# Kernel optimization log

Hardware: AMD Instinct MI355X
Metric: run time of the kernel (lower is better)

Reference implementation:

```python
import jax, jax.numpy as jnp
import numpy as np
from jax import lax

B, L, H = 2, 1024, 1024
D = 2048          # intermediate_size
N = 16            # ssm state size
K = 4             # conv kernel
R = 64            # time_step_rank


def setup_inputs() -> dict:
    key = jax.random.key(0)
    ks = jax.random.split(key, 10)
    def nrm(k, shape, scale=0.02):
        return jax.random.normal(k, shape, dtype=jnp.float32) * scale
    A = jnp.arange(1, N + 1, dtype=jnp.float32)[None, :] * jnp.ones((D, 1), jnp.float32)
    return {
        "hidden_states": jax.random.normal(ks[0], (B, L, H), dtype=jnp.float32),
        "W_in":  nrm(ks[1], (2 * D, H)),
        "conv_w": nrm(ks[2], (D, 1, K), 0.1),
        "conv_b": nrm(ks[3], (D,), 0.1),
        "W_x":   nrm(ks[4], (R + 2 * N, D)),
        "W_dt":  nrm(ks[5], (D, R), 0.1),
        "b_dt":  jnp.full((D,), -4.6, jnp.float32),  # softplus(-4.6) ~ 0.01 dt init
        "A_log": jnp.log(A),
        "D_param": jnp.ones((D,), jnp.float32),
        "W_out": nrm(ks[6], (H, D)),
    }


def _mamba_forward(hidden_states, W_in, conv_w, conv_b, W_x, W_dt, b_dt, A_log, D_param, W_out):
    silu = jax.nn.silu
    # in_proj -> [B, L, 2D], chunk into x and gate
    proj = jnp.einsum("blh,eh->ble", hidden_states, W_in)
    x, gate = jnp.split(proj, 2, axis=-1)           # [B,L,D] each
    # depthwise causal conv over time: [B,D,L]
    xc = x.swapaxes(1, 2)
    xc = lax.conv_general_dilated(
        xc, conv_w, window_strides=(1,), padding=[(K - 1, 0)],
        dimension_numbers=("NCH", "OIH", "NCH"), feature_group_count=D)
    x = silu(xc + conv_b[None, :, None]).swapaxes(1, 2)   # [B,L,D]
    # x_proj -> dt, Bmat, Cmat
    ssm_p = jnp.einsum("bld,rd->blr", x, W_x)             # [B,L,R+2N]
    dt_lr, Bm, Cm = ssm_p[..., :R], ssm_p[..., R:R + N], ssm_p[..., R + N:]
    dt = jax.nn.softplus(jnp.einsum("blr,dr->bld", dt_lr, W_dt) + b_dt)  # [B,L,D]
    A = -jnp.exp(A_log)                                   # [D,N]
    dA = jnp.exp(dt[..., None] * A[None, None])           # [B,L,D,N]
    dBu = dt[..., None] * Bm[:, :, None, :] * x[..., None]  # [B,L,D,N]
    # selective scan over time
    def step(h, inp):
        dA_t, dBu_t, C_t = inp                            # [B,D,N],[B,D,N],[B,N]
        h = dA_t * h + dBu_t
        y = jnp.einsum("bdn,bn->bd", h, C_t)
        return h, y
    h0 = jnp.zeros((B, D, N), dt.dtype)
    _, ys = lax.scan(step, h0, (dA.swapaxes(0, 1), dBu.swapaxes(0, 1), Cm.swapaxes(0, 1)))
    y = ys.swapaxes(0, 1)                                 # [B,L,D]
    y = (y + x * D_param[None, None, :]) * silu(gate)
    return jnp.einsum("bld,hd->blh", y, W_out)            # [B,L,H]


def reference(hidden_states, W_in, conv_w, conv_b, W_x, W_dt, b_dt, A_log, D_param, W_out):
    return _mamba_forward(hidden_states, W_in, conv_w, conv_b, W_x, W_dt, b_dt, A_log, D_param, W_out)
```

## Files before the change

kernel.cpp:

```cpp
#include <hip/hip_runtime.h>
#include <hip/hip_bf16.h>
#include <math.h>

#define B_ 2
#define L_ 1024
#define H_ 1024
#define D_ 2048
#define N_ 16
#define R_ 64
#define NCK 32
#define CL 32

typedef short short8 __attribute__((ext_vector_type(8)));
typedef float floatx4 __attribute__((ext_vector_type(4)));

__device__ __forceinline__ float siluf(float g) {
    return g / (1.0f + __expf(-g));
}

__device__ __forceinline__ unsigned short f2bf(float f) {
    unsigned int u = __float_as_uint(f);
    u = (u + 0x7fffu + ((u >> 16) & 1u)) >> 16;
    return (unsigned short)u;
}

__device__ __forceinline__ float bf2f(unsigned short u) {
    return __uint_as_float(((unsigned int)u) << 16);
}

__device__ __forceinline__ void gl2lds(const unsigned short* g, unsigned short* l) {
    __builtin_amdgcn_global_load_lds(
        (const __attribute__((address_space(1))) unsigned int*)g,
        (__attribute__((address_space(3))) unsigned int*)l, 16, 0, 0);
}

#define Q0 524288
#define Q1 1572864
#define Q2 2097152
#define Q3 2146304
#define Q4 2179072
__global__ __launch_bounds__(256) void cvt_all(
    const float* __restrict__ i0, const float* __restrict__ i1,
    const float* __restrict__ i2, const float* __restrict__ i3,
    const float* __restrict__ i4,
    unsigned short* __restrict__ o0, unsigned short* __restrict__ o1,
    unsigned short* __restrict__ o2, unsigned short* __restrict__ o3,
    unsigned short* __restrict__ o4)
{
    int q = blockIdx.x * 256 + threadIdx.x;
    if (q >= Q4) return;
    const float* in; unsigned short* out; int base;
    if (q < Q0)      { in = i0; out = o0; base = 0; }
    else if (q < Q1) { in = i1; out = o1; base = Q0; }
    else if (q < Q2) { in = i2; out = o2; base = Q1; }
    else if (q < Q3) { in = i3; out = o3; base = Q2; }
    else             { in = i4; out = o4; base = Q3; }
    int i = (q - base) * 4;
    float4 v = *(const float4*)(in + i);
    ushort4 o;
    o.x = f2bf(v.x); o.y = f2bf(v.y); o.z = f2bf(v.z); o.w = f2bf(v.w);
    *(ushort4*)(out + i) = o;
}

template<int EPI>
__global__ __launch_bounds__(256) void gemm_bf16_nt(
    const unsigned short* __restrict__ A, const unsigned short* __restrict__ Bm,
    float* __restrict__ C, int K, int Ncols, int ldc, int kChunk, int nMax,
    size_t partStride, unsigned short* __restrict__ C2)
{
    __shared__ unsigned short As[128 * 32];
    __shared__ unsigned short Bs[128 * 32];
    const int tid  = threadIdx.x;
    const int lane = tid & 63;
    const int wave = tid >> 6;
    const int wm = (wave >> 1) * 64;
    const int wn = (wave & 1) * 64;
    const int lr   = lane & 15;
    const int quad = lane >> 4;
    const int m0 = blockIdx.y * 128;
    const int n0 = blockIdx.x * 128;
    const int k0 = blockIdx.z * kChunk;

    const int srow = wave * 32 + (lane >> 2);
    const int sq   = (lane & 3) * 8;
    unsigned short* AsB0 = &As[(wave * 32) * 32];
    unsigned short* AsB1 = &As[(wave * 32 + 16) * 32];
    unsigned short* BsB0 = &Bs[(wave * 32) * 32];
    unsigned short* BsB1 = &Bs[(wave * 32 + 16) * 32];
    const size_t aoff0 = (size_t)(m0 + srow) * K + sq;
    const size_t aoff1 = (size_t)(m0 + srow + 16) * K + sq;
    const size_t boff0 = (size_t)min(n0 + srow, nMax - 1) * K + sq;
    const size_t boff1 = (size_t)min(n0 + srow + 16, nMax - 1) * K + sq;

    floatx4 acc[4][4];
#pragma unroll
    for (int mi = 0; mi < 4; ++mi)
#pragma unroll
        for (int ni = 0; ni < 4; ++ni)
            acc[mi][ni] = (floatx4){0.f, 0.f, 0.f, 0.f};

    for (int kt = k0; kt < k0 + kChunk; kt += 32) {
        __syncthreads();
        gl2lds(A + aoff0 + kt, AsB0);
        gl2lds(A + aoff1 + kt, AsB1);
        gl2lds(Bm + boff0 + kt, BsB0);
        gl2lds(Bm + boff1 + kt, BsB1);
        __syncthreads();
        short8 af[4], bf[4];
#pragma unroll
        for (int mi = 0; mi < 4; ++mi)
            af[mi] = *(const short8*)&As[(wm + mi * 16 + lr) * 32 + quad * 8];
#pragma unroll
        for (int ni = 0; ni < 4; ++ni)
            bf[ni] = *(const short8*)&Bs[(wn + ni * 16 + lr) * 32 + quad * 8];
#pragma unroll
        for (int mi = 0; mi < 4; ++mi)
#pragma unroll
            for (int ni = 0; ni < 4; ++ni)
                acc[mi][ni] = __builtin_amdgcn_mfma_f32_16x16x32_bf16(
                    af[mi], bf[ni], acc[mi][ni], 0, 0, 0);
    }

    if constexpr (EPI == 4) {
        if (n0 < 2048) {
            __shared__ unsigned short Ct[2 * 64 * 136];
            unsigned short* Cb = (unsigned short*)C;
            unsigned short* Cw = &Ct[(wave & 1) * 64 * 136];
#pragma unroll
            for (int mi = 0; mi < 4; ++mi)
#pragma unroll
                for (int ni = 0; ni < 4; ++ni) {
                    const int ccl = ni * 16 + lr;
                    const int rrl = wm + mi * 16 + quad * 4;
                    ushort4 v;
                    v.x = f2bf(acc[mi][ni][0]);
                    v.y = f2bf(acc[mi][ni][1]);
                    v.z = f2bf(acc[mi][ni][2]);
                    v.w = f2bf(acc[mi][ni][3]);
                    *(ushort4*)&Cw[ccl * 136 + rrl] = v;
                }
            __syncthreads();
            const int row = tid >> 2;
            const int mq = (tid & 3) * 32;
#pragma unroll
            for (int h = 0; h < 2; ++h) {
                const unsigned short* src = &Ct[h * 64 * 136 + row * 136 + mq];
                uint4 w0 = *(const uint4*)(src);
                uint4 w1 = *(const uint4*)(src + 8);
                uint4 w2 = *(const uint4*)(src + 16);
                uint4 w3 = *(const uint4*)(src + 24);
                unsigned short* dst = Cb + (size_t)(n0 + h * 64 + row) * 2048 + m0 + mq;
                *(uint4*)dst = w0;
                *(uint4*)(dst + 8) = w1;
                *(uint4*)(dst + 16) = w2;
                *(uint4*)(dst + 24) = w3;
            }
        } else {
#pragma unroll
            for (int mi = 0; mi < 4; ++mi)
#pragma unroll
                for (int ni = 0; ni < 4; ++ni) {
                    const int rr = m0 + wm + mi * 16 + quad * 4;
                    const int cc = n0 + wn + ni * 16 + lr - 2048;
#pragma unroll
                    for (int r = 0; r < 4; ++r)
                        C2[(size_t)(rr + r) * 2048 + cc] = f2bf(acc[mi][ni][r]);
                }
        }
    } else {
        float* Cz = C + (size_t)blockIdx.z * partStride;
#pragma unroll
        for (int mi = 0; mi < 4; ++mi)
#pragma unroll
            for (int ni = 0; ni < 4; ++ni) {
                const int rr = m0 + wm + mi * 16 + quad * 4;
                const int cc = n0 + wn + ni * 16 + lr;
                if (cc >= Ncols) continue;
#pragma unroll
                for (int r = 0; r < 4; ++r)
                    Cz[(size_t)(rr + r) * ldc + cc] = acc[mi][ni][r];
            }
    }
}

__global__ __launch_bounds__(256) void reduce_ssm(
    const float* __restrict__ P, float* __restrict__ ssm_p,
    unsigned short* __restrict__ sp64)
{
    const int q = blockIdx.x * 256 + threadIdx.x;
    const int m = q / 24;
    const int c = (q - m * 24) * 4;
    const size_t idx = (size_t)m * 96 + c;
    float4 s = make_float4(0.f, 0.f, 0.f, 0.f);
#pragma unroll
    for (int z = 0; z < 16; ++z) {
        float4 v = *(const float4*)(P + (size_t)z * (2048 * 96) + idx);
        s.x += v.x; s.y += v.y; s.z += v.z; s.w += v.w;
    }
    *(float4*)(ssm_p + idx) = s;
    if (c < 64) {
        ushort4 o;
        o.x = f2bf(s.x); o.y = f2bf(s.y); o.z = f2bf(s.z); o.w = f2bf(s.w);
        *(ushort4*)(sp64 + (size_t)m * 64 + c) = o;
    }
}

__global__ __launch_bounds__(256) void reduce_out(
    const float* __restrict__ P, float* __restrict__ out)
{
    const size_t i = ((size_t)blockIdx.x * 256 + threadIdx.x) * 4;
    float4 a = *(const float4*)(P + i);
    float4 b = *(const float4*)(P + 2097152 + i);
    float4 c = *(const float4*)(P + 2 * 2097152 + i);
    float4 d = *(const float4*)(P + 3 * 2097152 + i);
    *(float4*)(out + i) = make_float4(a.x + b.x + c.x + d.x,
                                      a.y + b.y + c.y + d.y,
                                      a.z + b.z + c.z + d.z,
                                      a.w + b.w + c.w + d.w);
}

__global__ __launch_bounds__(256) void dt_gemm(
    const unsigned short* __restrict__ A,
    const unsigned short* __restrict__ Bm,
    unsigned short* __restrict__ C,
    const float* __restrict__ bias)
{
    __shared__ unsigned short As[64 * 72];
    __shared__ unsigned short Bs[64 * 72];
    const int tid = threadIdx.x;
    const int lane = tid & 63;
    const int wave = tid >> 6;
    const int lr = lane & 15;
    const int quad = lane >> 4;
    const int n0 = blockIdx.x * 64;
    const int m0 = blockIdx.y * 64;

    {
        const int row = tid >> 3;
        const int cq = (tid & 7) * 8;
        uint4 a0 = *(const uint4*)(A + (size_t)(m0 + row) * 64 + cq);
        uint4 a1 = *(const uint4*)(A + (size_t)(m0 + 32 + row) * 64 + cq);
        uint4 b0 = *(const uint4*)(Bm + (size_t)(n0 + row) * 64 + cq);
        uint4 b1 = *(const uint4*)(Bm + (size_t)(n0 + 32 + row) * 64 + cq);
        *(uint4*)&As[row * 72 + cq] = a0;
        *(uint4*)&As[(32 + row) * 72 + cq] = a1;
        *(uint4*)&Bs[row * 72 + cq] = b0;
        *(uint4*)&Bs[(32 + row) * 72 + cq] = b1;
    }
    __syncthreads();

    floatx4 acc[4];
#pragma unroll
    for (int ni = 0; ni < 4; ++ni) acc[ni] = (floatx4){0.f, 0.f, 0.f, 0.f};

#pragma unroll
    for (int kt = 0; kt < 64; kt += 32) {
        short8 af = *(const short8*)&As[(wave * 16 + lr) * 72 + kt + quad * 8];
#pragma unroll
        for (int ni = 0; ni < 4; ++ni) {
            short8 bf = *(const short8*)&Bs[(ni * 16 + lr) * 72 + kt + quad * 8];
            acc[ni] = __builtin_amdgcn_mfma_f32_16x16x32_bf16(af, bf, acc[ni], 0, 0, 0);
        }
    }

    const int rr = m0 + wave * 16 + quad * 4;
#pragma unroll
    for (int ni = 0; ni < 4; ++ni) {
        const int cc = n0 + ni * 16 + lr;
        const float bv = bias[cc];
#pragma unroll
        for (int r = 0; r < 4; ++r) {
            const float z = acc[ni][r] + bv;
            const float spv = fmaxf(z, 0.f) + __logf(1.f + __expf(-fabsf(z)));
            C[(size_t)(rr + r) * 2048 + cc] = f2bf(spv);
        }
    }
}

__global__ __launch_bounds__(256) void conv_silu_kernel(
    const unsigned short* __restrict__ projx, const float* __restrict__ conv_w,
    const float* __restrict__ conv_b, unsigned short* __restrict__ x_bf)
{
    __shared__ unsigned short tile[64][72];
    const int t = threadIdx.x;
    const int d0 = blockIdx.x * 64;
    const int lt0 = blockIdx.y * 64;
    const int b = blockIdx.z;
    const int dl = t & 63;
    const int seg = t >> 6;
    const int d = d0 + dl;
    const int l0 = lt0 + seg * 16;
    const unsigned short* row = projx + (size_t)d * 2048 + b * 1024;
    const float w0 = conv_w[d * 4 + 0], w1 = conv_w[d * 4 + 1];
    const float w2 = conv_w[d * 4 + 2], w3 = conv_w[d * 4 + 3];
    const float bias = conv_b[d];

    float p[19];
    p[0] = (l0 >= 3) ? bf2f(row[l0 - 3]) : 0.f;
    p[1] = (l0 >= 2) ? bf2f(row[l0 - 2]) : 0.f;
    p[2] = (l0 >= 1) ? bf2f(row[l0 - 1]) : 0.f;
    {
        short8 q0 = *(const short8*)(row + l0);
        short8 q1 = *(const short8*)(row + l0 + 8);
#pragma unroll
        for (int j = 0; j < 8; ++j) {
            p[3 + j] = bf2f((unsigned short)q0[j]);
            p[11 + j] = bf2f((unsigned short)q1[j]);
        }
    }
#pragma unroll
    for (int j = 0; j < 16; ++j) {
        float v = siluf(bias + w0 * p[j] + w1 * p[j + 1] + w2 * p[j + 2] + w3 * p[j + 3]);
        tile[seg * 16 + j][dl] = f2bf(v);
    }
    __syncthreads();

    const int ml = t >> 2;
    const int c = t & 3;
    short8 s0 = *(const short8*)&tile[ml][c * 16];
    short8 s1 = *(const short8*)&tile[ml][c * 16 + 8];
    unsigned short* dst = x_bf + (size_t)(b * 1024 + lt0 + ml) * 2048 + d0 + c * 16;
    *(short8*)dst = s0;
    *(short8*)(dst + 8) = s1;
}

__global__ __launch_bounds__(256) void scan_p1(
    const unsigned short* __restrict__ dt, const unsigned short* __restrict__ x_bf,
    const float* __restrict__ sp, const float* __restrict__ A_log,
    float* __restrict__ Pch, float* __restrict__ Hch)
{
    __shared__ float sB[CL][16];
    const int tid = threadIdx.x;
    const int d = blockIdx.x * 256 + tid;
    const int ck = blockIdx.y;
    const int b = blockIdx.z;
    const int mb = b * 1024 + ck * CL;

    if (tid < CL * 4) {
        int row = tid >> 2, q = (tid & 3) * 4;
        *(float4*)&sB[row][q] = *(const float4*)(sp + (size_t)(mb + row) * 96 + 64 + q);
    }
    float An2[16];
    {
        const float* al = A_log + d * 16;
#pragma unroll
        for (int j = 0; j < 16; j += 4) {
            float4 a4 = *(const float4*)(al + j);
            An2[j + 0] = -__expf(a4.x) * 1.44269504f;
            An2[j + 1] = -__expf(a4.y) * 1.44269504f;
            An2[j + 2] = -__expf(a4.z) * 1.44269504f;
            An2[j + 3] = -__expf(a4.w) * 1.44269504f;
        }
    }
    __syncthreads();

    float h[16];
#pragma unroll
    for (int n = 0; n < 16; ++n) h[n] = 0.f;
    float dts = 0.f;

    for (int l = 0; l < CL; ++l) {
        const size_t off = (size_t)(mb + l) * 2048 + d;
        const float dtv = bf2f(dt[off]);
        const float xv = bf2f(x_bf[off]);
        const float u = dtv * xv;
        dts += dtv;
        float4 B0 = *(const float4*)&sB[l][0];
        float4 B1 = *(const float4*)&sB[l][4];
        float4 B2 = *(const float4*)&sB[l][8];
        float4 B3 = *(const float4*)&sB[l][12];
        float Bv[16] = {B0.x, B0.y, B0.z, B0.w, B1.x, B1.y, B1.z, B1.w,
                        B2.x, B2.y, B2.z, B2.w, B3.x, B3.y, B3.z, B3.w};
#pragma unroll
        for (int n = 0; n < 16; ++n) {
            const float dA = __builtin_amdgcn_exp2f(dtv * An2[n]);
            h[n] = fmaf(dA, h[n], Bv[n] * u);
        }
    }

    const size_t base = ((size_t)(b * NCK + ck) * 2048 + d) * 16;
#pragma unroll
    for (int j = 0; j < 16; j += 4) {
        float4 pv = make_float4(__builtin_amdgcn_exp2f(dts * An2[j]),
                                __builtin_amdgcn_exp2f(dts * An2[j + 1]),
                                __builtin_amdgcn_exp2f(dts * An2[j + 2]),
                                __builtin_amdgcn_exp2f(dts * An2[j + 3]));
        *(float4*)(Pch + base + j) = pv;
        *(float4*)(Hch + base + j) = make_float4(h[j], h[j + 1], h[j + 2], h[j + 3]);
    }
}

__global__ __launch_bounds__(256) void scan_combine(
    float* __restrict__ Pch, const float* __restrict__ Hch)
{
    const int flat = blockIdx.x * 256 + threadIdx.x;
    const int dn = flat & 32767;
    const int b = flat >> 15;
    float hin = 0.f;
#pragma unroll 4
    for (int ck = 0; ck < NCK; ++ck) {
        const size_t a = ((size_t)(b * NCK + ck) << 15) + dn;
        const float p = Pch[a];
        const float hc = Hch[a];
        Pch[a] = hin;
        hin = fmaf(p, hin, hc);
    }
}

__global__ __launch_bounds__(256) void scan_p2(
    const unsigned short* __restrict__ dt, const unsigned short* __restrict__ x_bf,
    const unsigned short* __restrict__ gate, const float* __restrict__ sp,
    const float* __restrict__ A_log, const float* __restrict__ Dp,
    const float* __restrict__ Hin, unsigned short* __restrict__ y_bf)
{
    __shared__ float sBC[CL][32];
    const int tid = threadIdx.x;
    const int d = blockIdx.x * 256 + tid;
    const int ck = blockIdx.y;
    const int b = blockIdx.z;
    const int mb = b * 1024 + ck * CL;

    {
        int row = tid >> 3, q = (tid & 7) * 4;
        *(float4*)&sBC[row][q] = *(const float4*)(sp + (size_t)(mb + row) * 96 + 64 + q);
    }
    float An2[16];
    {
        const float* al = A_log + d * 16;
#pragma unroll
        for (int j = 0; j < 16; j += 4) {
            float4 a4 = *(const float4*)(al + j);
            An2[j + 0] = -__expf(a4.x) * 1.44269504f;
            An2[j + 1] = -__expf(a4.y) * 1.44269504f;
            An2[j + 2] = -__expf(a4.z) * 1.44269504f;
            An2[j + 3] = -__expf(a4.w) * 1.44269504f;
        }
    }
    float h[16];
    {
        const size_t base = ((size_t)(b * NCK + ck) * 2048 + d) * 16;
#pragma unroll
        for (int j = 0; j < 16; j += 4) {
            float4 hv = *(const float4*)(Hin + base + j);
            h[j] = hv.x; h[j + 1] = hv.y; h[j + 2] = hv.z; h[j + 3] = hv.w;
        }
    }
    const float Dv = Dp[d];
    __syncthreads();

    for (int l = 0; l < CL; ++l) {
        const size_t off = (size_t)(mb + l) * 2048 + d;
        const float dtv = bf2f(dt[off]);
        const float xv = bf2f(x_bf[off]);
        const float gv = bf2f(gate[off]);
        const float u = dtv * xv;
        float4 B0 = *(const float4*)&sBC[l][0];
        float4 B1 = *(const float4*)&sBC[l][4];
        float4 B2 = *(const float4*)&sBC[l][8];
        float4 B3 = *(const float4*)&sBC[l][12];
        float Bv[16] = {B0.x, B0.y, B0.z, B0.w, B1.x, B1.y, B1.z, B1.w,
                        B2.x, B2.y, B2.z, B2.w, B3.x, B3.y, B3.z, B3.w};
#pragma unroll
        for (int n = 0; n < 16; ++n) {
            const float dA = __builtin_amdgcn_exp2f(dtv * An2[n]);
            h[n] = fmaf(dA, h[n], Bv[n] * u);
        }
        float4 C0 = *(const float4*)&sBC[l][16];
        float4 C1 = *(const float4*)&sBC[l][20];
        float4 C2 = *(const float4*)&sBC[l][24];
        float4 C3 = *(const float4*)&sBC[l][28];
        float Cv[16] = {C0.x, C0.y, C0.z, C0.w, C1.x, C1.y, C1.z, C1.w,
                        C2.x, C2.y, C2.z, C2.w, C3.x, C3.y, C3.z, C3.w};
        float p = 0.f;
#pragma unroll
        for (int n = 0; n < 16; ++n)
            p = fmaf(h[n], Cv[n], p);
        y_bf[off] = f2bf(fmaf(xv, Dv, p) * siluf(gv));
    }
}

extern "C" void kernel_launch(void* const* d_in, const int* in_sizes, int n_in,
                              void* d_out, int out_size, void* d_ws, size_t ws_size,
                              hipStream_t stream)
{
    const float* hs     = (const float*)d_in[0];
    const float* W_in   = (const float*)d_in[1];
    const float* conv_w = (const float*)d_in[2];
    const float* conv_b = (const float*)d_in[3];
    const float* W_x    = (const float*)d_in[4];
    const float* W_dt   = (const float*)d_in[5];
    const float* b_dt   = (const float*)d_in[6];
    const float* A_log  = (const float*)d_in[7];
    const float* Dp     = (const float*)d_in[8];
    const float* W_out  = (const float*)d_in[9];
    float* out = (float*)d_out;

    float* ws    = (float*)d_ws;
    float* gate_region = ws;
    float* dtb_region = gate_region + (size_t)4194304;
    float* projx_region = dtb_region + (size_t)4194304;
    float* ssm_p = projx_region + (size_t)4194304;
    unsigned short* hs_bf    = (unsigned short*)(ssm_p + 196608);
    unsigned short* W_in_bf  = hs_bf + (size_t)2097152;
    unsigned short* W_out_bf = W_in_bf + (size_t)4194304;
    unsigned short* W_x_bf   = W_out_bf + (size_t)2097152;
    unsigned short* W_dt_bf  = W_x_bf + (size_t)196608;
    unsigned short* sp64_bf  = W_dt_bf + (size_t)131072;
    unsigned short* x_bf     = sp64_bf + (size_t)131072;
    unsigned short* gate_bf  = (unsigned short*)gate_region;
    unsigned short* projx_bf = (unsigned short*)projx_region;
    unsigned short* dt_bf    = (unsigned short*)dtb_region;
    float* P1   = projx_region;
    float* Pch  = projx_region;
    float* Hch  = projx_region + (size_t)2097152;
    float* Pout = gate_region;
    unsigned short* y_bf = hs_bf;

    const int M = B_ * L_;

    cvt_all<<<(Q4 + 255) / 256, 256, 0, stream>>>(
        hs, W_in, W_out, W_x, W_dt, hs_bf, W_in_bf, W_out_bf, W_x_bf, W_dt_bf);

    gemm_bf16_nt<4><<<dim3(4096 / 128, M / 128, 1), 256, 0, stream>>>(
        hs_bf, W_in_bf, (float*)projx_bf, 1024, 4096, 2048, 1024, 4096, 0, gate_bf);

    conv_silu_kernel<<<dim3(D_ / 64, L_ / 64, B_), 256, 0, stream>>>(
        projx_bf, conv_w, conv_b, x_bf);

    gemm_bf16_nt<0><<<dim3(1, M / 128, 16), 256, 0, stream>>>(
        x_bf, W_x_bf, P1, 2048, 96, 96, 128, 96, (size_t)2048 * 96, nullptr);

    reduce_ssm<<<(2048 * 24) / 256, 256, 0, stream>>>(P1, ssm_p, sp64_bf);

    dt_gemm<<<dim3(2048 / 64, 2048 / 64), 256, 0, stream>>>(
        sp64_bf, W_dt_bf, dt_bf, b_dt);

    scan_p1<<<dim3(D_ / 256, NCK, B_), 256, 0, stream>>>(
        dt_bf, x_bf, ssm_p, A_log, Pch, Hch);
    scan_combine<<<(B_ * D_ * 16) / 256, 256, 0, stream>>>(Pch, Hch);
    scan_p2<<<dim3(D_ / 256, NCK, B_), 256, 0, stream>>>(
        dt_bf, x_bf, gate_bf, ssm_p, A_log, Dp, Pch, y_bf);

    gemm_bf16_nt<0><<<dim3(1024 / 128, M / 128, 4), 256, 0, stream>>>(
        y_bf, W_out_bf, Pout, 2048, 1024, 1024, 512, 1024, (size_t)2048 * 1024, nullptr);

    reduce_out<<<(2048 * 1024 / 4) / 256, 256, 0, stream>>>(Pout, out);
}
```

Before: 240.3 us.

## Fuse chunked scan into single kernel with decoupled flag-based chunk carry propagation

Replaces the three-kernel chunked selective scan (local pass, serial combine, second pass) with one kernel. Each block computes its chunk's local states and partial outputs in registers, publishes its chunk decay and state, then waits on release/acquire flags from earlier chunks to build the incoming state. The output is corrected using the cumulative decay times the carried-in state, so the second recurrence pass and the combine launch are no longer needed. In exchange it adds inter-block spin-waiting, which depends on all blocks being resident or scheduled in order, a memset for the flags, and higher register pressure from the fully unrolled per-step arrays.

```diff
diff --git a/kernel.cpp b/kernel.cpp
--- a/kernel.cpp
+++ b/kernel.cpp
@@ -324,21 +324,24 @@
     *(short8*)(dst + 8) = s1;
 }
 
-__global__ __launch_bounds__(256) void scan_p1(
+__global__ __launch_bounds__(256) void scan_one(
     const unsigned short* __restrict__ dt, const unsigned short* __restrict__ x_bf,
-    const float* __restrict__ sp, const float* __restrict__ A_log,
-    float* __restrict__ Pch, float* __restrict__ Hch)
-{
-    __shared__ float sB[CL][16];
+    const unsigned short* __restrict__ gate, const float* __restrict__ sp,
+    const float* __restrict__ A_log, const float* __restrict__ Dp,
+    float* __restrict__ Pagg, float* __restrict__ Hagg,
+    unsigned int* __restrict__ flags, unsigned short* __restrict__ y_bf)
+{
+    __shared__ float sBC[CL][32];
     const int tid = threadIdx.x;
-    const int d = blockIdx.x * 256 + tid;
+    const int dg = blockIdx.x;
+    const int d = dg * 256 + tid;
     const int ck = blockIdx.y;
     const int b = blockIdx.z;
     const int mb = b * 1024 + ck * CL;
 
-    if (tid < CL * 4) {
-        int row = tid >> 2, q = (tid & 3) * 4;
-        *(float4*)&sB[row][q] = *(const float4*)(sp + (size_t)(mb + row) * 96 + 64 + q);
+    {
+        int row = tid >> 3, q = (tid & 7) * 4;
+        *(float4*)&sBC[row][q] = *(const float4*)(sp + (size_t)(mb + row) * 96 + 64 + q);
     }
     float An2[16];
     {
@@ -357,125 +360,95 @@
     float h[16];
 #pragma unroll
     for (int n = 0; n < 16; ++n) h[n] = 0.f;
+    float cumdt[CL], psum[CL];
     float dts = 0.f;
-
+#pragma unroll
     for (int l = 0; l < CL; ++l) {
         const size_t off = (size_t)(mb + l) * 2048 + d;
         const float dtv = bf2f(dt[off]);
         const float xv = bf2f(x_bf[off]);
         const float u = dtv * xv;
         dts += dtv;
-        float4 B0 = *(const float4*)&sB[l][0];
-        float4 B1 = *(const float4*)&sB[l][4];
-        float4 B2 = *(const float4*)&sB[l][8];
-        float4 B3 = *(const float4*)&sB[l][12];
+        cumdt[l] = dts;
+        float4 B0 = *(const float4*)&sBC[l][0];
+        float4 B1 = *(const float4*)&sBC[l][4];
+        float4 B2 = *(const float4*)&sBC[l][8];
+        float4 B3 = *(const float4*)&sBC[l][12];
+        float4 C0 = *(const float4*)&sBC[l][16];
+        float4 C1 = *(const float4*)&sBC[l][20];
+        float4 C2 = *(const float4*)&sBC[l][24];
+        float4 C3 = *(const float4*)&sBC[l][28];
         float Bv[16] = {B0.x, B0.y, B0.z, B0.w, B1.x, B1.y, B1.z, B1.w,
                         B2.x, B2.y, B2.z, B2.w, B3.x, B3.y, B3.z, B3.w};
+        float Cv[16] = {C0.x, C0.y, C0.z, C0.w, C1.x, C1.y, C1.z, C1.w,
+                        C2.x, C2.y, C2.z, C2.w, C3.x, C3.y, C3.z, C3.w};
+        float ps = 0.f;
 #pragma unroll
         for (int n = 0; n < 16; ++n) {
             const float dA = __builtin_amdgcn_exp2f(dtv * An2[n]);
             h[n] = fmaf(dA, h[n], Bv[n] * u);
-        }
-    }
-
-    const size_t base = ((size_t)(b * NCK + ck) * 2048 + d) * 16;
+            ps = fmaf(h[n], Cv[n], ps);
+        }
+        psum[l] = ps;
+    }
+
+    const size_t abase = ((size_t)(b * NCK + ck) * 2048 + d) * 16;
 #pragma unroll
     for (int j = 0; j < 16; j += 4) {
         float4 pv = make_float4(__builtin_amdgcn_exp2f(dts * An2[j]),
                                 __builtin_amdgcn_exp2f(dts * An2[j + 1]),
                                 __builtin_amdgcn_exp2f(dts * An2[j + 2]),
                                 __builtin_amdgcn_exp2f(dts * An2[j + 3]));
-        *(float4*)(Pch + base + j) = pv;
-        *(float4*)(Hch + base + j) = make_float4(h[j], h[j + 1], h[j + 2], h[j + 3]);
-    }
-}
-
-__global__ __launch_bounds__(256) void scan_combine(
-    float* __restrict__ Pch, const float* __restrict__ Hch)
-{
-    const int flat = blockIdx.x * 256 + threadIdx.x;
-    const int dn = flat & 32767;
-    const int b = flat >> 15;
-    float hin = 0.f;
-#pragma unroll 4
-    for (int ck = 0; ck < NCK; ++ck) {
-        const size_t a = ((size_t)(b * NCK + ck) << 15) + dn;
-        const float p = Pch[a];
-        const float hc = Hch[a];
-        Pch[a] = hin;
-        hin = fmaf(p, hin, hc);
-    }
-}
-
-__global__ __launch_bounds__(256) void scan_p2(
-    const unsigned short* __restrict__ dt, const unsigned short* __restrict__ x_bf,
-    const unsigned short* __restrict__ gate, const float* __restrict__ sp,
-    const float* __restrict__ A_log, const float* __restrict__ Dp,
-    const float* __restrict__ Hin, unsigned short* __restrict__ y_bf)
-{
-    __shared__ float sBC[CL][32];
-    const int tid = threadIdx.x;
-    const int d = blockIdx.x * 256 + tid;
-    const int ck = blockIdx.y;
-    const int b = blockIdx.z;
-    const int mb = b * 1024 + ck * CL;
-
-    {
-        int row = tid >> 3, q = (tid & 7) * 4;
-        *(float4*)&sBC[row][q] = *(const float4*)(sp + (size_t)(mb + row) * 96 + 64 + q);
-    }
-    float An2[16];
-    {
-        const float* al = A_log + d * 16;
-#pragma unroll
-        for (int j = 0; j < 16; j += 4) {
-            float4 a4 = *(const float4*)(al + j);
-            An2[j + 0] = -__expf(a4.x) * 1.44269504f;
-            An2[j + 1] = -__expf(a4.y) * 1.44269504f;
-            An2[j + 2] = -__expf(a4.z) * 1.44269504f;
-            An2[j + 3] = -__expf(a4.w) * 1.44269504f;
-        }
-    }
-    float h[16];
-    {
-        const size_t base = ((size_t)(b * NCK + ck) * 2048 + d) * 16;
-#pragma unroll
-        for (int j = 0; j < 16; j += 4) {
-            float4 hv = *(const float4*)(Hin + base + j);
-            h[j] = hv.x; h[j + 1] = hv.y; h[j + 2] = hv.z; h[j + 3] = hv.w;
-        }
-    }
+        *(float4*)(Pagg + abase + j) = pv;
+        *(float4*)(Hagg + abase + j) = make_float4(h[j], h[j + 1], h[j + 2], h[j + 3]);
+    }
+    __threadfence();
+    __syncthreads();
+    if (tid == 0)
+        __hip_atomic_store(&flags[(b * NCK + ck) * 8 + dg], 1u,
+                           __ATOMIC_RELEASE, __HIP_MEMORY_SCOPE_AGENT);
+
+    float hin[16];
+#pragma unroll
+    for (int n = 0; n < 16; ++n) hin[n] = 0.f;
+    for (int j = 0; j < ck; ++j) {
+        if (tid == 0) {
+            while (__hip_atomic_load(&flags[(b * NCK + j) * 8 + dg],
+                                     __ATOMIC_ACQUIRE, __HIP_MEMORY_SCOPE_AGENT) == 0) {
+                __builtin_amdgcn_s_sleep(8);
+            }
+        }
+        __syncthreads();
+        const size_t jb = ((size_t)(b * NCK + j) * 2048 + d) * 16;
+#pragma unroll
+        for (int q = 0; q < 16; q += 4) {
+            float4 P4 = *(const float4*)(Pagg + jb + q);
+            float4 H4 = *(const float4*)(Hagg + jb + q);
+            hin[q + 0] = fmaf(P4.x, hin[q + 0], H4.x);
+            hin[q + 1] = fmaf(P4.y, hin[q + 1], H4.y);
+            hin[q + 2] = fmaf(P4.z, hin[q + 2], H4.z);
+            hin[q + 3] = fmaf(P4.w, hin[q + 3], H4.w);
+        }
+    }
+
     const float Dv = Dp[d];
-    __syncthreads();
-
+#pragma unroll
     for (int l = 0; l < CL; ++l) {
         const size_t off = (size_t)(mb + l) * 2048 + d;
-        const float dtv = bf2f(dt[off]);
         const float xv = bf2f(x_bf[off]);
         const float gv = bf2f(gate[off]);
-        const float u = dtv * xv;
-        float4 B0 = *(const float4*)&sBC[l][0];
-        float4 B1 = *(const float4*)&sBC[l][4];
-        float4 B2 = *(const float4*)&sBC[l][8];
-        float4 B3 = *(const float4*)&sBC[l][12];
-        float Bv[16] = {B0.x, B0.y, B0.z, B0.w, B1.x, B1.y, B1.z, B1.w,
-                        B2.x, B2.y, B2.z, B2.w, B3.x, B3.y, B3.z, B3.w};
-#pragma unroll
-        for (int n = 0; n < 16; ++n) {
-            const float dA = __builtin_amdgcn_exp2f(dtv * An2[n]);
-            h[n] = fmaf(dA, h[n], Bv[n] * u);
-        }
         float4 C0 = *(const float4*)&sBC[l][16];
         float4 C1 = *(const float4*)&sBC[l][20];
         float4 C2 = *(const float4*)&sBC[l][24];
         float4 C3 = *(const float4*)&sBC[l][28];
         float Cv[16] = {C0.x, C0.y, C0.z, C0.w, C1.x, C1.y, C1.z, C1.w,
                         C2.x, C2.y, C2.z, C2.w, C3.x, C3.y, C3.z, C3.w};
-        float p = 0.f;
+        float corr = 0.f;
+        const float cd = cumdt[l];
 #pragma unroll
         for (int n = 0; n < 16; ++n)
-            p = fmaf(h[n], Cv[n], p);
-        y_bf[off] = f2bf(fmaf(xv, Dv, p) * siluf(gv));
+            corr = fmaf(__builtin_amdgcn_exp2f(cd * An2[n]) * Cv[n], hin[n], corr);
+        y_bf[off] = f2bf((psum[l] + corr + xv * Dv) * siluf(gv));
     }
 }
 
@@ -511,8 +484,9 @@
     unsigned short* projx_bf = (unsigned short*)projx_region;
     unsigned short* dt_bf    = (unsigned short*)dtb_region;
     float* P1   = projx_region;
-    float* Pch  = projx_region;
-    float* Hch  = projx_region + (size_t)2097152;
+    float* Pagg = projx_region;
+    float* Hagg = projx_region + (size_t)2097152;
+    unsigned int* flags = (unsigned int*)(dtb_region + (size_t)2097152);
     float* Pout = gate_region;
     unsigned short* y_bf = hs_bf;
 
@@ -535,11 +509,9 @@
     dt_gemm<<<dim3(2048 / 64, 2048 / 64), 256, 0, stream>>>(
         sp64_bf, W_dt_bf, dt_bf, b_dt);
 
-    scan_p1<<<dim3(D_ / 256, NCK, B_), 256, 0, stream>>>(
-        dt_bf, x_bf, ssm_p, A_log, Pch, Hch);
-    scan_combine<<<(B_ * D_ * 16) / 256, 256, 0, stream>>>(Pch, Hch);
-    scan_p2<<<dim3(D_ / 256, NCK, B_), 256, 0, stream>>>(
-        dt_bf, x_bf, gate_bf, ssm_p, A_log, Dp, Pch, y_bf);
+    hipMemsetAsync(flags, 0, 512 * sizeof(unsigned int), stream);
+    scan_one<<<dim3(D_ / 256, NCK, B_), 256, 0, stream>>>(
+        dt_bf, x_bf, gate_bf, ssm_p, A_log, Dp, Pagg, Hagg, flags, y_bf);
 
     gemm_bf16_nt<0><<<dim3(1024 / 128, M / 128, 4), 256, 0, stream>>>(
         y_bf, W_out_bf, Pout, 2048, 1024, 1024, 512, 1024, (size_t)2048 * 1024, nullptr);
```

Measured after the change: 789.0 us. 228% more time.
